# Kernel optimization log

Hardware: AMD Instinct MI355X
Metric: run time of the kernel (lower is better)

## Reference

```python
import jax, jax.numpy as jnp
import numpy as np

D = 512   # dense write dimension
M = 64    # number of experts
B = 16    # per-expert sparse code width
N = 8192  # tokens
K = 4     # experts per token (top-k)


def _normalize_U(U):
    # UnitColNormPadded(dim=1): each column of the (D+1, b) expert matrix
    # is rescaled to unit L2 norm along the padded (D+1) axis.
    nrm = jnp.sqrt(jnp.sum(U * U, axis=1, keepdims=True))
    return U / nrm


def setup_inputs() -> dict:
    key = jax.random.key(0)
    k1, k2, k3 = jax.random.split(key, 3)
    h_sparse = jax.random.normal(k1, (N, K, B), dtype=jnp.float32)
    topk_idxs = jax.random.randint(k2, (N, K), 0, M)
    U = jax.random.normal(k3, (M, D + 1, B), dtype=jnp.float32)
    return {"h_sparse": h_sparse, "topk_idxs": topk_idxs, "U": U}


def reference(h_sparse, topk_idxs, U):
    Un = _normalize_U(U)                      # (m, D+1, b)
    U_active = Un[topk_idxs][:, :, :D, :]     # gather -> (N, k, D, b)
    writes = jnp.einsum('nkdb,nkb->nd', U_active, h_sparse)   # (N, D)
    h_recon = jnp.einsum('nkdb,nd->nkb', U_active, writes)    # (N, k, b)
    h_target = jax.lax.stop_gradient(h_sparse)
    diff = h_recon - h_target
    writer_aux_loss = jnp.mean(diff * diff)
    return writes, writer_aux_loss
```

## Files before the change

### kernel.cpp

```cpp
#include <hip/hip_runtime.h>

#define DD 512
#define MM 64
#define BB 16
#define NN 8192
#define KK 4
#define DP1 513
#define CAP 1024
#define NPAIR (NN * KK)

#define CNT_B  0
#define BKT_B  33024
#define U_B    164096
#define UT_B   1212672
#define WBF_B  2261248
#define PART_B 10649856
#define WS_NEED 44204288

typedef unsigned int uint;
typedef unsigned short ushort;
typedef __attribute__((ext_vector_type(8))) short short8;
typedef __attribute__((ext_vector_type(4))) float f32x4;

__device__ __forceinline__ ushort f2bf(float f) {
    uint u = __builtin_bit_cast(uint, f);
    uint r = (u + 0x7FFFu + ((u >> 16) & 1u)) >> 16;
    return (ushort)r;
}
__device__ __forceinline__ float bf2f(ushort s) {
    return __builtin_bit_cast(float, (uint)s << 16);
}

__global__ __launch_bounds__(256) void prep_build(
    const float* __restrict__ U,
    const int*   __restrict__ topk,
    void* __restrict__ ws,
    float* __restrict__ loss_slot)
{
    const int blk = blockIdx.x, t = threadIdx.x;

    if (blk < 256) {
        const int m = blk >> 2, sl = blk & 3;
        const float* Um = U + (long)m * DP1 * BB;

        __shared__ float red[256];
        __shared__ float inv_s[BB];
        __shared__ ushort tr[BB][136];

        float a = 0.f;
        for (int i = t; i < DP1 * BB; i += 256) { float v = Um[i]; a += v * v; }
        red[t] = a;
        __syncthreads();
        if (t < BB) {
            float tot = 0.f;
            #pragma unroll
            for (int j = 0; j < 16; ++j) tot += red[t + 16 * j];
            inv_s[t] = rsqrtf(tot);
        }
        __syncthreads();

        ushort* ub = (ushort*)((char*)ws + U_B) + (long)m * DD * BB + sl * 2048;
        ushort* ut = (ushort*)((char*)ws + UT_B) + (long)m * BB * DD + sl * 128;
        const float* Us = Um + sl * 2048;

        #pragma unroll
        for (int iter = 0; iter < 4; ++iter) {
            const int i = t + iter * 256;
            const int e0 = 2 * i;
            const int dl = e0 >> 4, b0 = e0 & 15;
            const float2 v = *(const float2*)(Us + e0);
            const ushort bv0 = f2bf(v.x * inv_s[b0]);
            const ushort bv1 = f2bf(v.y * inv_s[b0 + 1]);
            *(uint*)(ub + e0) = (uint)bv0 | ((uint)bv1 << 16);
            tr[b0][dl]     = bv0;
            tr[b0 + 1][dl] = bv1;
        }
        __syncthreads();
        {
            const int b = t >> 4, doff = (t & 15) * 8;
            uint4 val;
            val.x = (uint)tr[b][doff + 0] | ((uint)tr[b][doff + 1] << 16);
            val.y = (uint)tr[b][doff + 2] | ((uint)tr[b][doff + 3] << 16);
            val.z = (uint)tr[b][doff + 4] | ((uint)tr[b][doff + 5] << 16);
            val.w = (uint)tr[b][doff + 6] | ((uint)tr[b][doff + 7] << 16);
            *(uint4*)(ut + (long)b * DD + doff) = val;
        }
    } else {
        const int cblk = blk - 256;
        int* cnt = (int*)ws;
        ushort* bkt = (ushort*)((char*)ws + BKT_B);
        __shared__ int lc[MM], lb[MM];
        if (t < MM) lc[t] = 0;
        __syncthreads();
        const int p = cblk * 256 + t;
        const int e = topk[p];
        const int my = atomicAdd(&lc[e], 1);
        __syncthreads();
        if (t < MM) lb[t] = atomicAdd(&cnt[t], lc[t]);
        __syncthreads();
        bkt[e * CAP + lb[e] + my] = (ushort)p;
        if (cblk == 0 && t == 0) *loss_slot = 0.f;
    }
}

__global__ __launch_bounds__(256) void pass_writes_mfma(
    const float* __restrict__ h_sparse, void* __restrict__ ws)
{
    const int e = blockIdx.x & 63, g = blockIdx.x >> 6;
    const int wave = threadIdx.x >> 6, lane = threadIdx.x & 63;
    const int quad = lane >> 4, l15 = lane & 15;

    const int* cnt = (const int*)ws;
    const ushort* bkt = (const ushort*)((const char*)ws + BKT_B);
    const ushort* Ue = (const ushort*)((const char*)ws + U_B) + (long)e * DD * BB;
    ushort* part = (ushort*)((char*)ws + PART_B);

    const int c  = cnt[e];
    const int lo = (c * g) >> 3;
    const int hi = (c * (g + 1)) >> 3;

    for (int base = lo + wave * 16; base < hi; base += 64) {
        const int pidx = base + l15;
        const bool valid = pidx < hi;
        const int id = valid ? (int)bkt[e * CAP + pidx] : 0;
        const int n = id >> 2, k = id & 3;

        short8 bfrag = (short8)0;
        if (quad < 2 && valid) {
            const float4* hp = (const float4*)(h_sparse + (long)id * BB + quad * 8);
            const float4 h0 = hp[0], h1 = hp[1];
            bfrag[0] = (short)f2bf(h0.x); bfrag[1] = (short)f2bf(h0.y);
            bfrag[2] = (short)f2bf(h0.z); bfrag[3] = (short)f2bf(h0.w);
            bfrag[4] = (short)f2bf(h1.x); bfrag[5] = (short)f2bf(h1.y);
            bfrag[6] = (short)f2bf(h1.z); bfrag[7] = (short)f2bf(h1.w);
        }
        ushort* prow = part + ((long)(k * NN + n) << 9);

        #pragma unroll 2
        for (int dt = 0; dt < 32; dt += 2) {
            short8 a0 = (short8)0, a1 = (short8)0;
            if (quad < 2) {
                a0 = *(const short8*)(Ue + ((long)(dt * 16 + l15) << 4) + quad * 8);
                a1 = *(const short8*)(Ue + ((long)((dt + 1) * 16 + l15) << 4) + quad * 8);
            }
            f32x4 z = {0.f, 0.f, 0.f, 0.f};
            f32x4 c0 = __builtin_amdgcn_mfma_f32_16x16x32_bf16(a0, bfrag, z, 0, 0, 0);
            f32x4 c1 = __builtin_amdgcn_mfma_f32_16x16x32_bf16(a1, bfrag, z, 0, 0, 0);

            uint p0x = (uint)f2bf(c0[0]) | ((uint)f2bf(c0[1]) << 16);
            uint p0y = (uint)f2bf(c0[2]) | ((uint)f2bf(c0[3]) << 16);
            uint p1x = (uint)f2bf(c1[0]) | ((uint)f2bf(c1[1]) << 16);
            uint p1y = (uint)f2bf(c1[2]) | ((uint)f2bf(c1[3]) << 16);
            uint q0x = __shfl_xor((int)p0x, 16, 64);
            uint q0y = __shfl_xor((int)p0y, 16, 64);
            uint q1x = __shfl_xor((int)p1x, 16, 64);
            uint q1y = __shfl_xor((int)p1y, 16, 64);

            if (valid) {
                uint4 st;
                int sdt;
                if ((quad & 1) == 0) { st.x = p0x; st.y = p0y; st.z = q0x; st.w = q0y; sdt = dt; }
                else                 { st.x = q1x; st.y = q1y; st.z = p1x; st.w = p1y; sdt = dt + 1; }
                const int srow = (quad & 2) ? 8 : 0;
                *(uint4*)(prow + sdt * 16 + srow) = st;
            }
        }
    }
}

__global__ __launch_bounds__(256) void reduce_w(
    void* __restrict__ ws, float* __restrict__ out)
{
    const uint4* part4 = (const uint4*)((const char*)ws + PART_B);
    uint4* wbf4 = (uint4*)((char*)ws + WBF_B);
    const int gsz = NN * DD / 8;
    const int gid = blockIdx.x * 256 + threadIdx.x;

    const uint4 v0 = part4[gid];
    const uint4 v1 = part4[(long)gsz + gid];
    const uint4 v2 = part4[2L * gsz + gid];
    const uint4 v3 = part4[3L * gsz + gid];

    float s[8];
    s[0] = bf2f((ushort)v0.x) + bf2f((ushort)v1.x) + bf2f((ushort)v2.x) + bf2f((ushort)v3.x);
    s[1] = bf2f((ushort)(v0.x >> 16)) + bf2f((ushort)(v1.x >> 16)) + bf2f((ushort)(v2.x >> 16)) + bf2f((ushort)(v3.x >> 16));
    s[2] = bf2f((ushort)v0.y) + bf2f((ushort)v1.y) + bf2f((ushort)v2.y) + bf2f((ushort)v3.y);
    s[3] = bf2f((ushort)(v0.y >> 16)) + bf2f((ushort)(v1.y >> 16)) + bf2f((ushort)(v2.y >> 16)) + bf2f((ushort)(v3.y >> 16));
    s[4] = bf2f((ushort)v0.z) + bf2f((ushort)v1.z) + bf2f((ushort)v2.z) + bf2f((ushort)v3.z);
    s[5] = bf2f((ushort)(v0.z >> 16)) + bf2f((ushort)(v1.z >> 16)) + bf2f((ushort)(v2.z >> 16)) + bf2f((ushort)(v3.z >> 16));
    s[6] = bf2f((ushort)v0.w) + bf2f((ushort)v1.w) + bf2f((ushort)v2.w) + bf2f((ushort)v3.w);
    s[7] = bf2f((ushort)(v0.w >> 16)) + bf2f((ushort)(v1.w >> 16)) + bf2f((ushort)(v2.w >> 16)) + bf2f((ushort)(v3.w >> 16));

    float4* out4 = (float4*)out;
    out4[(long)gid * 2 + 0] = make_float4(s[0], s[1], s[2], s[3]);
    out4[(long)gid * 2 + 1] = make_float4(s[4], s[5], s[6], s[7]);

    uint4 pk;
    pk.x = (uint)f2bf(s[0]) | ((uint)f2bf(s[1]) << 16);
    pk.y = (uint)f2bf(s[2]) | ((uint)f2bf(s[3]) << 16);
    pk.z = (uint)f2bf(s[4]) | ((uint)f2bf(s[5]) << 16);
    pk.w = (uint)f2bf(s[6]) | ((uint)f2bf(s[7]) << 16);
    wbf4[gid] = pk;
}

__global__ __launch_bounds__(256) void pass_recon_mfma(
    const float* __restrict__ h_sparse, void* __restrict__ ws,
    float* __restrict__ out)
{
    const int e = blockIdx.x & 63, g = blockIdx.x >> 6;
    const int wave = threadIdx.x >> 6, lane = threadIdx.x & 63;
    const int quad = lane >> 4, l15 = lane & 15;
    const int t = threadIdx.x;

    const int* cnt = (const int*)ws;
    const ushort* bkt = (const ushort*)((const char*)ws + BKT_B);
    const ushort* Ute = (const ushort*)((const char*)ws + UT_B) + (long)e * BB * DD;
    const ushort* wbf = (const ushort*)((const char*)ws + WBF_B);

    __shared__ float loss_blk;
    if (t == 0) loss_blk = 0.f;
    __syncthreads();

    const int c  = cnt[e];
    const int lo = (c * g) >> 3;
    const int hi = (c * (g + 1)) >> 3;

    float lsum = 0.f;
    for (int base = lo + wave * 16; base < hi; base += 64) {
        const int pidx = base + l15;
        const bool valid = pidx < hi;
        const int id = valid ? (int)bkt[e * CAP + pidx] : 0;
        const int n = id >> 2;
        const ushort* wrow = wbf + ((long)n << 9);

        f32x4 acc = {0.f, 0.f, 0.f, 0.f};
        #pragma unroll 4
        for (int kk = 0; kk < 16; ++kk) {
            const int doff = kk * 32 + quad * 8;
            const short8 afrag = *(const short8*)(wrow + doff);
            const short8 bfrag = *(const short8*)(Ute + (long)l15 * DD + doff);
            acc = __builtin_amdgcn_mfma_f32_16x16x32_bf16(afrag, bfrag, acc, 0, 0, 0);
        }
        #pragma unroll
        for (int r = 0; r < 4; ++r) {
            const int pr = base + quad * 4 + r;
            if (pr < hi) {
                const int id2 = (int)bkt[e * CAP + pr];
                const float h = h_sparse[(long)id2 * BB + l15];
                const float d = acc[r] - h;
                lsum += d * d;
            }
        }
    }
    #pragma unroll
    for (int off = 32; off > 0; off >>= 1) lsum += __shfl_xor(lsum, off, 64);
    if (lane == 0 && lsum != 0.f) atomicAdd(&loss_blk, lsum);
    __syncthreads();
    if (t == 0 && loss_blk != 0.f)
        atomicAdd(out + (long)NN * DD, loss_blk * (1.0f / ((float)NN * KK * BB)));
}

__global__ __launch_bounds__(256) void norm_kernel(
    const float* __restrict__ U, float* __restrict__ inv_norm,
    float* __restrict__ loss_slot)
{
    const int m = blockIdx.x;
    const int t = threadIdx.x;
    const float* Um = U + (long)m * DP1 * BB;
    float acc = 0.f;
    for (int idx = t; idx < DP1 * BB; idx += 256) {
        float v = Um[idx];
        acc += v * v;
    }
    __shared__ float s[256];
    s[t] = acc;
    __syncthreads();
    if (t < BB) {
        float tot = 0.f;
        #pragma unroll
        for (int j = 0; j < 16; ++j) tot += s[t + 16 * j];
        inv_norm[m * BB + t] = rsqrtf(tot);
    }
    if (m == 0 && t == 0) *loss_slot = 0.f;
}

__global__ __launch_bounds__(256) void dense_write_kernel(
    const float* __restrict__ h_sparse,
    const int*   __restrict__ topk,
    const float* __restrict__ U,
    const float* __restrict__ inv_norm,
    float* __restrict__ out)
{
    const int n = blockIdx.x;
    const int t = threadIdx.x;

    __shared__ float hs[KK * BB];
    __shared__ float ho[KK * BB];
    __shared__ float inv_s[KK * BB];
    __shared__ int   eidx[KK];
    __shared__ float w_s[DD];
    __shared__ float red[256];

    if (t < KK) eidx[t] = topk[n * KK + t];
    __syncthreads();
    if (t < KK * BB) {
        const int k = t / BB, b = t % BB;
        const float h  = h_sparse[(long)n * KK * BB + t];
        const float iv = inv_norm[eidx[k] * BB + b];
        ho[t]    = h;
        inv_s[t] = iv;
        hs[t]    = h * iv;
    }
    __syncthreads();

    #pragma unroll
    for (int dd = 0; dd < 2; ++dd) {
        const int d = t + dd * 256;
        float w = 0.f;
        #pragma unroll
        for (int k = 0; k < KK; ++k) {
            const float4* row = (const float4*)(U + ((long)eidx[k] * DP1 + d) * BB);
            #pragma unroll
            for (int q = 0; q < 4; ++q) {
                const float4 u4 = row[q];
                w += u4.x * hs[k * BB + 4 * q + 0];
                w += u4.y * hs[k * BB + 4 * q + 1];
                w += u4.z * hs[k * BB + 4 * q + 2];
                w += u4.w * hs[k * BB + 4 * q + 3];
            }
        }
        w_s[d] = w;
        out[(long)n * DD + d] = w;
    }
    __syncthreads();

    {
        const int pair = t & 63;
        const int k = pair >> 4, b = pair & 15;
        const int ch = t >> 6;
        const float* Ucol = U + (long)eidx[k] * DP1 * BB + b;
        float p = 0.f;
        #pragma unroll 8
        for (int d = ch * 128; d < ch * 128 + 128; ++d) {
            p += Ucol[(long)d * BB] * w_s[d];
        }
        red[t] = p;
    }
    __syncthreads();

    if (t < 64) {
        const float recon = (red[t] + red[t + 64] + red[t + 128] + red[t + 192]) * inv_s[t];
        const float diff  = recon - ho[t];
        float sq = diff * diff;
        #pragma unroll
        for (int off = 32; off > 0; off >>= 1) sq += __shfl_down(sq, off, 64);
        if (t == 0) {
            atomicAdd(out + (long)NN * DD, sq * (1.0f / ((float)NN * KK * BB)));
        }
    }
}


extern "C" void kernel_launch(void* const* d_in, const int* in_sizes, int n_in,
                              void* d_out, int out_size, void* d_ws, size_t ws_size,
                              hipStream_t stream) {
    const float* h_sparse = (const float*)d_in[0];
    const int*   topk     = (const int*)d_in[1];
    const float* U        = (const float*)d_in[2];
    float* out = (float*)d_out;

    if (ws_size >= (size_t)WS_NEED) {
        hipMemsetAsync(d_ws, 0, 256, stream);
        hipLaunchKernelGGL(prep_build, dim3(256 + NPAIR / 256), dim3(256), 0, stream,
                           U, topk, d_ws, out + (long)NN * DD);
        hipLaunchKernelGGL(pass_writes_mfma, dim3(MM * 8), dim3(256), 0, stream,
                           h_sparse, d_ws);
        hipLaunchKernelGGL(reduce_w, dim3(NN * DD / 8 / 256), dim3(256), 0, stream,
                           d_ws, out);
        hipLaunchKernelGGL(pass_recon_mfma, dim3(MM * 8), dim3(256), 0, stream,
                           h_sparse, d_ws, out);
    } else {
        float* inv_norm = (float*)d_ws;
        hipLaunchKernelGGL(norm_kernel, dim3(MM), dim3(256), 0, stream,
                           U, inv_norm, out + (long)NN * DD);
        hipLaunchKernelGGL(dense_write_kernel, dim3(NN), dim3(256), 0, stream,
                           h_sparse, topk, U, inv_norm, out);
    }
}
```

Baseline: 125.5 us.

## Compute reconstruction loss via expert Gram matrices instead of re-reading writes

Replaces the reconstruction pass, which re-read the full bf16 writes matrix per token-expert pair, with precomputed 64x64 blocks of 16x16 expert Gram matrices (U_e^T U_f). The Gram blocks are built by extra blocks in the writes kernel, and the loss is computed inside the reduce kernel from the Gram entries and h_sparse. This removes one kernel launch, the bf16 writes buffer store and the large gather reads. The cost is a Gram table of about 4 MB, whose entries are fetched per token, and a change in rounding for the loss.

```diff
diff --git a/kernel.cpp b/kernel.cpp
--- a/kernel.cpp
+++ b/kernel.cpp
@@ -13,7 +13,7 @@
 #define BKT_B  33024
 #define U_B    164096
 #define UT_B   1212672
-#define WBF_B  2261248
+#define GRAM_B 2261248
 #define PART_B 10649856
 #define WS_NEED 44204288
 
@@ -106,158 +106,168 @@
 __global__ __launch_bounds__(256) void pass_writes_mfma(
     const float* __restrict__ h_sparse, void* __restrict__ ws)
 {
-    const int e = blockIdx.x & 63, g = blockIdx.x >> 6;
     const int wave = threadIdx.x >> 6, lane = threadIdx.x & 63;
     const int quad = lane >> 4, l15 = lane & 15;
 
-    const int* cnt = (const int*)ws;
-    const ushort* bkt = (const ushort*)((const char*)ws + BKT_B);
-    const ushort* Ue = (const ushort*)((const char*)ws + U_B) + (long)e * DD * BB;
-    ushort* part = (ushort*)((char*)ws + PART_B);
-
-    const int c  = cnt[e];
-    const int lo = (c * g) >> 3;
-    const int hi = (c * (g + 1)) >> 3;
-
-    for (int base = lo + wave * 16; base < hi; base += 64) {
-        const int pidx = base + l15;
-        const bool valid = pidx < hi;
-        const int id = valid ? (int)bkt[e * CAP + pidx] : 0;
-        const int n = id >> 2, k = id & 3;
-
-        short8 bfrag = (short8)0;
-        if (quad < 2 && valid) {
-            const float4* hp = (const float4*)(h_sparse + (long)id * BB + quad * 8);
-            const float4 h0 = hp[0], h1 = hp[1];
-            bfrag[0] = (short)f2bf(h0.x); bfrag[1] = (short)f2bf(h0.y);
-            bfrag[2] = (short)f2bf(h0.z); bfrag[3] = (short)f2bf(h0.w);
-            bfrag[4] = (short)f2bf(h1.x); bfrag[5] = (short)f2bf(h1.y);
-            bfrag[6] = (short)f2bf(h1.z); bfrag[7] = (short)f2bf(h1.w);
-        }
-        ushort* prow = part + ((long)(k * NN + n) << 9);
-
-        #pragma unroll 2
-        for (int dt = 0; dt < 32; dt += 2) {
-            short8 a0 = (short8)0, a1 = (short8)0;
-            if (quad < 2) {
-                a0 = *(const short8*)(Ue + ((long)(dt * 16 + l15) << 4) + quad * 8);
-                a1 = *(const short8*)(Ue + ((long)((dt + 1) * 16 + l15) << 4) + quad * 8);
+    if (blockIdx.x < MM * 8) {
+        const int e = blockIdx.x & 63, g = blockIdx.x >> 6;
+
+        const int* cnt = (const int*)ws;
+        const ushort* bkt = (const ushort*)((const char*)ws + BKT_B);
+        const ushort* Ue = (const ushort*)((const char*)ws + U_B) + (long)e * DD * BB;
+        ushort* part = (ushort*)((char*)ws + PART_B);
+
+        const int c  = cnt[e];
+        const int lo = (c * g) >> 3;
+        const int hi = (c * (g + 1)) >> 3;
+
+        for (int base = lo + wave * 16; base < hi; base += 64) {
+            const int pidx = base + l15;
+            const bool valid = pidx < hi;
+            const int id = valid ? (int)bkt[e * CAP + pidx] : 0;
+            const int n = id >> 2, k = id & 3;
+
+            short8 bfrag = (short8)0;
+            if (quad < 2 && valid) {
+                const float4* hp = (const float4*)(h_sparse + (long)id * BB + quad * 8);
+                const float4 h0 = hp[0], h1 = hp[1];
+                bfrag[0] = (short)f2bf(h0.x); bfrag[1] = (short)f2bf(h0.y);
+                bfrag[2] = (short)f2bf(h0.z); bfrag[3] = (short)f2bf(h0.w);
+                bfrag[4] = (short)f2bf(h1.x); bfrag[5] = (short)f2bf(h1.y);
+                bfrag[6] = (short)f2bf(h1.z); bfrag[7] = (short)f2bf(h1.w);
             }
-            f32x4 z = {0.f, 0.f, 0.f, 0.f};
-            f32x4 c0 = __builtin_amdgcn_mfma_f32_16x16x32_bf16(a0, bfrag, z, 0, 0, 0);
-            f32x4 c1 = __builtin_amdgcn_mfma_f32_16x16x32_bf16(a1, bfrag, z, 0, 0, 0);
-
-            uint p0x = (uint)f2bf(c0[0]) | ((uint)f2bf(c0[1]) << 16);
-            uint p0y = (uint)f2bf(c0[2]) | ((uint)f2bf(c0[3]) << 16);
-            uint p1x = (uint)f2bf(c1[0]) | ((uint)f2bf(c1[1]) << 16);
-            uint p1y = (uint)f2bf(c1[2]) | ((uint)f2bf(c1[3]) << 16);
-            uint q0x = __shfl_xor((int)p0x, 16, 64);
-            uint q0y = __shfl_xor((int)p0y, 16, 64);
-            uint q1x = __shfl_xor((int)p1x, 16, 64);
-            uint q1y = __shfl_xor((int)p1y, 16, 64);
-
-            if (valid) {
-                uint4 st;
-                int sdt;
-                if ((quad & 1) == 0) { st.x = p0x; st.y = p0y; st.z = q0x; st.w = q0y; sdt = dt; }
-                else                 { st.x = q1x; st.y = q1y; st.z = p1x; st.w = p1y; sdt = dt + 1; }
-                const int srow = (quad & 2) ? 8 : 0;
-                *(uint4*)(prow + sdt * 16 + srow) = st;
+            ushort* prow = part + ((long)(k * NN + n) << 9);
+
+            #pragma unroll 2
+            for (int dt = 0; dt < 32; dt += 2) {
+                short8 a0 = (short8)0, a1 = (short8)0;
+                if (quad < 2) {
+                    a0 = *(const short8*)(Ue + ((long)(dt * 16 + l15) << 4) + quad * 8);
+                    a1 = *(const short8*)(Ue + ((long)((dt + 1) * 16 + l15) << 4) + quad * 8);
+                }
+                f32x4 z = {0.f, 0.f, 0.f, 0.f};
+                f32x4 c0 = __builtin_amdgcn_mfma_f32_16x16x32_bf16(a0, bfrag, z, 0, 0, 0);
+                f32x4 c1 = __builtin_amdgcn_mfma_f32_16x16x32_bf16(a1, bfrag, z, 0, 0, 0);
+
+                uint p0x = (uint)f2bf(c0[0]) | ((uint)f2bf(c0[1]) << 16);
+                uint p0y = (uint)f2bf(c0[2]) | ((uint)f2bf(c0[3]) << 16);
+                uint p1x = (uint)f2bf(c1[0]) | ((uint)f2bf(c1[1]) << 16);
+                uint p1y = (uint)f2bf(c1[2]) | ((uint)f2bf(c1[3]) << 16);
+                uint q0x = __shfl_xor((int)p0x, 16, 64);
+                uint q0y = __shfl_xor((int)p0y, 16, 64);
+                uint q1x = __shfl_xor((int)p1x, 16, 64);
+                uint q1y = __shfl_xor((int)p1y, 16, 64);
+
+                if (valid) {
+                    uint4 st;
+                    int sdt;
+                    if ((quad & 1) == 0) { st.x = p0x; st.y = p0y; st.z = q0x; st.w = q0y; sdt = dt; }
+                    else                 { st.x = q1x; st.y = q1y; st.z = p1x; st.w = p1y; sdt = dt + 1; }
+                    const int srow = (quad & 2) ? 8 : 0;
+                    *(uint4*)(prow + sdt * 16 + srow) = st;
+                }
             }
         }
+    } else {
+        const int gblk = blockIdx.x - MM * 8;
+        const int e = gblk >> 4;
+        const int f = (gblk & 15) * 4 + wave;
+
+        const ushort* utp = (const ushort*)((const char*)ws + UT_B);
+        const ushort* ue = utp + (long)e * BB * DD + (long)l15 * DD + quad * 8;
+        const ushort* uf = utp + (long)f * BB * DD + (long)l15 * DD + quad * 8;
+
+        f32x4 acc = {0.f, 0.f, 0.f, 0.f};
+        #pragma unroll
+        for (int dblk = 0; dblk < 16; ++dblk) {
+            const short8 a = *(const short8*)(ue + dblk * 32);
+            const short8 b = *(const short8*)(uf + dblk * 32);
+            acc = __builtin_amdgcn_mfma_f32_16x16x32_bf16(a, b, acc, 0, 0, 0);
+        }
+        float* G = (float*)((char*)ws + GRAM_B) + (((long)e * MM + f) << 8);
+        #pragma unroll
+        for (int r = 0; r < 4; ++r)
+            G[(quad * 4 + r) * 16 + l15] = acc[r];
     }
 }
 
 __global__ __launch_bounds__(256) void reduce_w(
+    const float* __restrict__ h_sparse,
+    const int*   __restrict__ topk,
     void* __restrict__ ws, float* __restrict__ out)
 {
-    const uint4* part4 = (const uint4*)((const char*)ws + PART_B);
-    uint4* wbf4 = (uint4*)((char*)ws + WBF_B);
-    const int gsz = NN * DD / 8;
-    const int gid = blockIdx.x * 256 + threadIdx.x;
-
-    const uint4 v0 = part4[gid];
-    const uint4 v1 = part4[(long)gsz + gid];
-    const uint4 v2 = part4[2L * gsz + gid];
-    const uint4 v3 = part4[3L * gsz + gid];
-
-    float s[8];
-    s[0] = bf2f((ushort)v0.x) + bf2f((ushort)v1.x) + bf2f((ushort)v2.x) + bf2f((ushort)v3.x);
-    s[1] = bf2f((ushort)(v0.x >> 16)) + bf2f((ushort)(v1.x >> 16)) + bf2f((ushort)(v2.x >> 16)) + bf2f((ushort)(v3.x >> 16));
-    s[2] = bf2f((ushort)v0.y) + bf2f((ushort)v1.y) + bf2f((ushort)v2.y) + bf2f((ushort)v3.y);
-    s[3] = bf2f((ushort)(v0.y >> 16)) + bf2f((ushort)(v1.y >> 16)) + bf2f((ushort)(v2.y >> 16)) + bf2f((ushort)(v3.y >> 16));
-    s[4] = bf2f((ushort)v0.z) + bf2f((ushort)v1.z) + bf2f((ushort)v2.z) + bf2f((ushort)v3.z);
-    s[5] = bf2f((ushort)(v0.z >> 16)) + bf2f((ushort)(v1.z >> 16)) + bf2f((ushort)(v2.z >> 16)) + bf2f((ushort)(v3.z >> 16));
-    s[6] = bf2f((ushort)v0.w) + bf2f((ushort)v1.w) + bf2f((ushort)v2.w) + bf2f((ushort)v3.w);
-    s[7] = bf2f((ushort)(v0.w >> 16)) + bf2f((ushort)(v1.w >> 16)) + bf2f((ushort)(v2.w >> 16)) + bf2f((ushort)(v3.w >> 16));
-
-    float4* out4 = (float4*)out;
-    out4[(long)gid * 2 + 0] = make_float4(s[0], s[1], s[2], s[3]);
-    out4[(long)gid * 2 + 1] = make_float4(s[4], s[5], s[6], s[7]);
-
-    uint4 pk;
-    pk.x = (uint)f2bf(s[0]) | ((uint)f2bf(s[1]) << 16);
-    pk.y = (uint)f2bf(s[2]) | ((uint)f2bf(s[3]) << 16);
-    pk.z = (uint)f2bf(s[4]) | ((uint)f2bf(s[5]) << 16);
-    pk.w = (uint)f2bf(s[6]) | ((uint)f2bf(s[7]) << 16);
-    wbf4[gid] = pk;
-}
-
-__global__ __launch_bounds__(256) void pass_recon_mfma(
-    const float* __restrict__ h_sparse, void* __restrict__ ws,
-    float* __restrict__ out)
-{
-    const int e = blockIdx.x & 63, g = blockIdx.x >> 6;
-    const int wave = threadIdx.x >> 6, lane = threadIdx.x & 63;
-    const int quad = lane >> 4, l15 = lane & 15;
     const int t = threadIdx.x;
 
-    const int* cnt = (const int*)ws;
-    const ushort* bkt = (const ushort*)((const char*)ws + BKT_B);
-    const ushort* Ute = (const ushort*)((const char*)ws + UT_B) + (long)e * BB * DD;
-    const ushort* wbf = (const ushort*)((const char*)ws + WBF_B);
-
-    __shared__ float loss_blk;
-    if (t == 0) loss_blk = 0.f;
-    __syncthreads();
-
-    const int c  = cnt[e];
-    const int lo = (c * g) >> 3;
-    const int hi = (c * (g + 1)) >> 3;
-
-    float lsum = 0.f;
-    for (int base = lo + wave * 16; base < hi; base += 64) {
-        const int pidx = base + l15;
-        const bool valid = pidx < hi;
-        const int id = valid ? (int)bkt[e * CAP + pidx] : 0;
-        const int n = id >> 2;
-        const ushort* wrow = wbf + ((long)n << 9);
-
-        f32x4 acc = {0.f, 0.f, 0.f, 0.f};
-        #pragma unroll 4
-        for (int kk = 0; kk < 16; ++kk) {
-            const int doff = kk * 32 + quad * 8;
-            const short8 afrag = *(const short8*)(wrow + doff);
-            const short8 bfrag = *(const short8*)(Ute + (long)l15 * DD + doff);
-            acc = __builtin_amdgcn_mfma_f32_16x16x32_bf16(afrag, bfrag, acc, 0, 0, 0);
-        }
-        #pragma unroll
-        for (int r = 0; r < 4; ++r) {
-            const int pr = base + quad * 4 + r;
-            if (pr < hi) {
-                const int id2 = (int)bkt[e * CAP + pr];
-                const float h = h_sparse[(long)id2 * BB + l15];
-                const float d = acc[r] - h;
-                lsum += d * d;
+    if (blockIdx.x < NN * DD / 8 / 256) {
+        const uint4* part4 = (const uint4*)((const char*)ws + PART_B);
+        const int gsz = NN * DD / 8;
+        const int gid = blockIdx.x * 256 + t;
+
+        const uint4 v0 = part4[gid];
+        const uint4 v1 = part4[(long)gsz + gid];
+        const uint4 v2 = part4[2L * gsz + gid];
+        const uint4 v3 = part4[3L * gsz + gid];
+
+        float s[8];
+        s[0] = bf2f((ushort)v0.x) + bf2f((ushort)v1.x) + bf2f((ushort)v2.x) + bf2f((ushort)v3.x);
+        s[1] = bf2f((ushort)(v0.x >> 16)) + bf2f((ushort)(v1.x >> 16)) + bf2f((ushort)(v2.x >> 16)) + bf2f((ushort)(v3.x >> 16));
+        s[2] = bf2f((ushort)v0.y) + bf2f((ushort)v1.y) + bf2f((ushort)v2.y) + bf2f((ushort)v3.y);
+        s[3] = bf2f((ushort)(v0.y >> 16)) + bf2f((ushort)(v1.y >> 16)) + bf2f((ushort)(v2.y >> 16)) + bf2f((ushort)(v3.y >> 16));
+        s[4] = bf2f((ushort)v0.z) + bf2f((ushort)v1.z) + bf2f((ushort)v2.z) + bf2f((ushort)v3.z);
+        s[5] = bf2f((ushort)(v0.z >> 16)) + bf2f((ushort)(v1.z >> 16)) + bf2f((ushort)(v2.z >> 16)) + bf2f((ushort)(v3.z >> 16));
+        s[6] = bf2f((ushort)v0.w) + bf2f((ushort)v1.w) + bf2f((ushort)v2.w) + bf2f((ushort)v3.w);
+        s[7] = bf2f((ushort)(v0.w >> 16)) + bf2f((ushort)(v1.w >> 16)) + bf2f((ushort)(v2.w >> 16)) + bf2f((ushort)(v3.w >> 16));
+
+        float4* out4 = (float4*)out;
+        out4[(long)gid * 2 + 0] = make_float4(s[0], s[1], s[2], s[3]);
+        out4[(long)gid * 2 + 1] = make_float4(s[4], s[5], s[6], s[7]);
+    } else {
+        const int lb = blockIdx.x - NN * DD / 8 / 256;
+        const int wave = t >> 6, lane = t & 63;
+        const int quad = lane >> 4, l15 = lane & 15;
+        const float* G = (const float*)((const char*)ws + GRAM_B);
+
+        __shared__ float loss_blk;
+        if (t == 0) loss_blk = 0.f;
+        __syncthreads();
+
+        float lsum = 0.f;
+        const int wgid = lb * 4 + wave;
+        for (int i = 0; i < 8; ++i) {
+            const int n = __builtin_amdgcn_readfirstlane(wgid * 8 + i);
+            const int4 tk = *(const int4*)(topk + n * 4);
+            const int ek = quad == 0 ? tk.x : quad == 1 ? tk.y : quad == 2 ? tk.z : tk.w;
+            const float* hn = h_sparse + (long)n * (KK * BB);
+
+            float recon = 0.f;
+            #pragma unroll
+            for (int j = 0; j < 4; ++j) {
+                const int ej = j == 0 ? tk.x : j == 1 ? tk.y : j == 2 ? tk.z : tk.w;
+                const float* Grow = G + (((long)(ek * MM + ej)) << 8) + l15 * 16;
+                const float4 g0 = *(const float4*)(Grow + 0);
+                const float4 g1 = *(const float4*)(Grow + 4);
+                const float4 g2 = *(const float4*)(Grow + 8);
+                const float4 g3 = *(const float4*)(Grow + 12);
+                const float4 h0 = *(const float4*)(hn + j * 16 + 0);
+                const float4 h1 = *(const float4*)(hn + j * 16 + 4);
+                const float4 h2 = *(const float4*)(hn + j * 16 + 8);
+                const float4 h3 = *(const float4*)(hn + j * 16 + 12);
+                recon += g0.x * h0.x + g0.y * h0.y + g0.z * h0.z + g0.w * h0.w;
+                recon += g1.x * h1.x + g1.y * h1.y + g1.z * h1.z + g1.w * h1.w;
+                recon += g2.x * h2.x + g2.y * h2.y + g2.z * h2.z + g2.w * h2.w;
+                recon += g3.x * h3.x + g3.y * h3.y + g3.z * h3.z + g3.w * h3.w;
             }
-        }
-    }
-    #pragma unroll
-    for (int off = 32; off > 0; off >>= 1) lsum += __shfl_xor(lsum, off, 64);
-    if (lane == 0 && lsum != 0.f) atomicAdd(&loss_blk, lsum);
-    __syncthreads();
-    if (t == 0 && loss_blk != 0.f)
-        atomicAdd(out + (long)NN * DD, loss_blk * (1.0f / ((float)NN * KK * BB)));
+            const float hv = hn[quad * 16 + l15];
+            const float d = recon - hv;
+            lsum += d * d;
+        }
+        #pragma unroll
+        for (int off = 32; off > 0; off >>= 1) lsum += __shfl_xor(lsum, off, 64);
+        if (lane == 0 && lsum != 0.f) atomicAdd(&loss_blk, lsum);
+        __syncthreads();
+        if (t == 0 && loss_blk != 0.f)
+            atomicAdd(out + (long)NN * DD, loss_blk * (1.0f / ((float)NN * KK * BB)));
+    }
 }
 
 __global__ __launch_bounds__(256) void norm_kernel(
@@ -373,12 +383,10 @@
         hipMemsetAsync(d_ws, 0, 256, stream);
         hipLaunchKernelGGL(prep_build, dim3(256 + NPAIR / 256), dim3(256), 0, stream,
                            U, topk, d_ws, out + (long)NN * DD);
-        hipLaunchKernelGGL(pass_writes_mfma, dim3(MM * 8), dim3(256), 0, stream,
+        hipLaunchKernelGGL(pass_writes_mfma, dim3(MM * 8 + MM * 16), dim3(256), 0, stream,
                            h_sparse, d_ws);
-        hipLaunchKernelGGL(reduce_w, dim3(NN * DD / 8 / 256), dim3(256), 0, stream,
-                           d_ws, out);
-        hipLaunchKernelGGL(pass_recon_mfma, dim3(MM * 8), dim3(256), 0, stream,
-                           h_sparse, d_ws, out);
+        hipLaunchKernelGGL(reduce_w, dim3(NN * DD / 8 / 256 + 256), dim3(256), 0, stream,
+                           h_sparse, topk, d_ws, out);
     } else {
         float* inv_norm = (float*)d_ws;
         hipLaunchKernelGGL(norm_kernel, dim3(MM), dim3(256), 0, stream,
```

Result: slower. 132.5 us (+5.5%).

## Split expert work across more blocks and pair waves over D halves

Applied to the files above, without the earlier changes.

Both MFMA passes now split each expert's bucket into 16 groups instead of 8, and the grids double to 1024 blocks. Within a block, waves work in pairs: in the writes pass each wave handles half of the D tiles, and in the recon pass each handles half of the K reduction. The recon halves are combined through shared memory with barriers. This targets low occupancy and poor load balance on a large-CU GPU, at the cost of extra syncthreads and duplicated h_sparse/bucket loads.

```diff
diff --git a/kernel.cpp b/kernel.cpp
--- a/kernel.cpp
+++ b/kernel.cpp
@@ -109,6 +109,7 @@
     const int e = blockIdx.x & 63, g = blockIdx.x >> 6;
     const int wave = threadIdx.x >> 6, lane = threadIdx.x & 63;
     const int quad = lane >> 4, l15 = lane & 15;
+    const int wp = wave >> 1, half = wave & 1;
 
     const int* cnt = (const int*)ws;
     const ushort* bkt = (const ushort*)((const char*)ws + BKT_B);
@@ -116,10 +117,10 @@
     ushort* part = (ushort*)((char*)ws + PART_B);
 
     const int c  = cnt[e];
-    const int lo = (c * g) >> 3;
-    const int hi = (c * (g + 1)) >> 3;
-
-    for (int base = lo + wave * 16; base < hi; base += 64) {
+    const int lo = (c * g) >> 4;
+    const int hi = (c * (g + 1)) >> 4;
+
+    for (int base = lo + wp * 16; base < hi; base += 32) {
         const int pidx = base + l15;
         const bool valid = pidx < hi;
         const int id = valid ? (int)bkt[e * CAP + pidx] : 0;
@@ -136,8 +137,9 @@
         }
         ushort* prow = part + ((long)(k * NN + n) << 9);
 
+        const int dt0 = half * 16;
         #pragma unroll 2
-        for (int dt = 0; dt < 32; dt += 2) {
+        for (int dt = dt0; dt < dt0 + 16; dt += 2) {
             short8 a0 = (short8)0, a1 = (short8)0;
             if (quad < 2) {
                 a0 = *(const short8*)(Ue + ((long)(dt * 16 + l15) << 4) + quad * 8);
@@ -210,6 +212,7 @@
     const int e = blockIdx.x & 63, g = blockIdx.x >> 6;
     const int wave = threadIdx.x >> 6, lane = threadIdx.x & 63;
     const int quad = lane >> 4, l15 = lane & 15;
+    const int wp = wave >> 1, half = wave & 1;
     const int t = threadIdx.x;
 
     const int* cnt = (const int*)ws;
@@ -218,39 +221,59 @@
     const ushort* wbf = (const ushort*)((const char*)ws + WBF_B);
 
     __shared__ float loss_blk;
+    __shared__ float4 accsh[2][64];
     if (t == 0) loss_blk = 0.f;
     __syncthreads();
 
     const int c  = cnt[e];
-    const int lo = (c * g) >> 3;
-    const int hi = (c * (g + 1)) >> 3;
+    const int lo = (c * g) >> 4;
+    const int hi = (c * (g + 1)) >> 4;
+
+    const int tiles = (hi - lo + 15) >> 4;
+    const int maxiter = (tiles + 1) >> 1;
 
     float lsum = 0.f;
-    for (int base = lo + wave * 16; base < hi; base += 64) {
-        const int pidx = base + l15;
-        const bool valid = pidx < hi;
-        const int id = valid ? (int)bkt[e * CAP + pidx] : 0;
-        const int n = id >> 2;
-        const ushort* wrow = wbf + ((long)n << 9);
+    for (int it = 0; it < maxiter; ++it) {
+        const int ti = it * 2 + wp;
+        const int base = lo + ti * 16;
+        const bool active = ti < tiles;
 
         f32x4 acc = {0.f, 0.f, 0.f, 0.f};
-        #pragma unroll 4
-        for (int kk = 0; kk < 16; ++kk) {
-            const int doff = kk * 32 + quad * 8;
-            const short8 afrag = *(const short8*)(wrow + doff);
-            const short8 bfrag = *(const short8*)(Ute + (long)l15 * DD + doff);
-            acc = __builtin_amdgcn_mfma_f32_16x16x32_bf16(afrag, bfrag, acc, 0, 0, 0);
-        }
-        #pragma unroll
-        for (int r = 0; r < 4; ++r) {
-            const int pr = base + quad * 4 + r;
-            if (pr < hi) {
-                const int id2 = (int)bkt[e * CAP + pr];
-                const float h = h_sparse[(long)id2 * BB + l15];
-                const float d = acc[r] - h;
-                lsum += d * d;
+        int id = 0;
+        if (active) {
+            const int pidx = base + l15;
+            const bool valid = pidx < hi;
+            id = valid ? (int)bkt[e * CAP + pidx] : 0;
+            const int n = id >> 2;
+            const ushort* wrow = wbf + ((long)n << 9);
+
+            const int kk0 = half * 8;
+            #pragma unroll 4
+            for (int kk = kk0; kk < kk0 + 8; ++kk) {
+                const int doff = kk * 32 + quad * 8;
+                const short8 afrag = *(const short8*)(wrow + doff);
+                const short8 bfrag = *(const short8*)(Ute + (long)l15 * DD + doff);
+                acc = __builtin_amdgcn_mfma_f32_16x16x32_bf16(afrag, bfrag, acc, 0, 0, 0);
             }
         }
+        if (half == 1)
+            accsh[wp][lane] = make_float4(acc[0], acc[1], acc[2], acc[3]);
+        __syncthreads();
+        if (half == 0 && active) {
+            const float4 o = accsh[wp][lane];
+            acc[0] += o.x; acc[1] += o.y; acc[2] += o.z; acc[3] += o.w;
+            #pragma unroll
+            for (int r = 0; r < 4; ++r) {
+                const int pr = base + quad * 4 + r;
+                if (pr < hi) {
+                    const int id2 = (int)bkt[e * CAP + pr];
+                    const float h = h_sparse[(long)id2 * BB + l15];
+                    const float d = acc[r] - h;
+                    lsum += d * d;
+                }
+            }
+        }
+        __syncthreads();
     }
     #pragma unroll
     for (int off = 32; off > 0; off >>= 1) lsum += __shfl_xor(lsum, off, 64);
@@ -373,11 +396,11 @@
         hipMemsetAsync(d_ws, 0, 256, stream);
         hipLaunchKernelGGL(prep_build, dim3(256 + NPAIR / 256), dim3(256), 0, stream,
                            U, topk, d_ws, out + (long)NN * DD);
-        hipLaunchKernelGGL(pass_writes_mfma, dim3(MM * 8), dim3(256), 0, stream,
+        hipLaunchKernelGGL(pass_writes_mfma, dim3(MM * 16), dim3(256), 0, stream,
                            h_sparse, d_ws);
         hipLaunchKernelGGL(reduce_w, dim3(NN * DD / 8 / 256), dim3(256), 0, stream,
                            d_ws, out);
-        hipLaunchKernelGGL(pass_recon_mfma, dim3(MM * 8), dim3(256), 0, stream,
+        hipLaunchKernelGGL(pass_recon_mfma, dim3(MM * 16), dim3(256), 0, stream,
                            h_sparse, d_ws, out);
     } else {
         float* inv_norm = (float*)d_ws;
```

New measurement: 127.3 us. No clear change (+1.4%).
